# Performance work log

Hardware: AMD Instinct MI355X
Metric: run time of the kernel (lower is better)

The kernel has to match this reference:

```python
import jax, jax.numpy as jnp
import numpy as np

B, T, D = 2, 2048, 2048
H, HKV, RD = 16, 4, 64
DH = D // H          # 128
REP = H // HKV       # 4
NEG = -1e30


def _apply_rope(x, cos, sin, rd):
    # x: (B, h, T, Dh); cos/sin: (T, rd//2) broadcast over (B, h)
    xr, xp = x[..., :rd], x[..., rd:]
    x1, x2 = xr[..., ::2], xr[..., 1::2]
    rot = jnp.stack([x1 * cos - x2 * sin, x1 * sin + x2 * cos], axis=-1)
    rot = rot.reshape(x1.shape[:-1] + (rd,))
    return jnp.concatenate([rot, xp], axis=-1)


def setup_inputs() -> dict:
    key = jax.random.key(0)
    ks = jax.random.split(key, 6)
    x = jax.random.normal(ks[0], (B, T, D), dtype=jnp.float32)
    # rotary tables for the first RD dims (RD//2 frequency pairs)
    inv_freq = 1.0 / (10000.0 ** (np.arange(RD // 2, dtype=np.float32) / (RD // 2)))
    ang = np.arange(T, dtype=np.float32)[:, None] * inv_freq[None, :]  # (T, RD//2)
    cos = jnp.asarray(np.cos(ang), dtype=jnp.float32)
    sin = jnp.asarray(np.sin(ang), dtype=jnp.float32)
    s = 0.02
    Wq = jax.random.normal(ks[1], (H * DH, D), dtype=jnp.float32) * s
    Wk = jax.random.normal(ks[2], (HKV * DH, D), dtype=jnp.float32) * s
    Wv = jax.random.normal(ks[3], (HKV * DH, D), dtype=jnp.float32) * s
    Wo = jax.random.normal(ks[4], (D, D), dtype=jnp.float32) * s
    temp = jnp.full((H,), 1.0 / np.sqrt(DH), dtype=jnp.float32)
    return {"x": x, "cos": cos, "sin": sin, "Wq": Wq, "Wk": Wk, "Wv": Wv, "Wo": Wo, "temp": temp}


def reference(x, cos, sin, Wq, Wk, Wv, Wo, temp):
    Bt, Tt, _ = x.shape
    q = (x @ Wq.T).reshape(Bt, Tt, H, DH).transpose(0, 2, 1, 3)    # (B,H,T,Dh)
    k = (x @ Wk.T).reshape(Bt, Tt, HKV, DH).transpose(0, 2, 1, 3)  # (B,Hkv,T,Dh)
    v = (x @ Wv.T).reshape(Bt, Tt, HKV, DH).transpose(0, 2, 1, 3)
    k = jnp.repeat(k, REP, axis=1)  # GQA repeat_interleave -> (B,H,T,Dh)
    v = jnp.repeat(v, REP, axis=1)
    q = _apply_rope(q, cos, sin, RD)
    k = _apply_rope(k, cos, sin, RD)
    q = q * temp[None, :, None, None]
    # SDPA causal, with default 1/sqrt(Dh) scale on top of learned temp
    scores = jnp.einsum("bhqd,bhkd->bhqk", q, k) / np.sqrt(DH)
    causal = jnp.tril(jnp.ones((Tt, Tt), dtype=bool))
    scores = jnp.where(causal[None, None], scores, NEG)
    attn = jax.nn.softmax(scores, axis=-1)
    out = jnp.einsum("bhqk,bhkd->bhqd", attn, v)  # (B,H,T,Dh)
    out = out.transpose(0, 2, 1, 3).reshape(Bt, Tt, H * DH)
    return out @ Wo.T
```

## Files before the change

kernel.cpp:

```cpp
#include <hip/hip_runtime.h>
#include <hip/hip_bf16.h>
#include <math.h>

#define B_   2
#define T_   2048
#define D_   2048
#define H_   16
#define HKV_ 4
#define DH_  128
#define RD_  64
#define KD_  (HKV_ * DH_)
#define SQKV 3072
#define VOFF 2560

typedef __attribute__((ext_vector_type(8))) short  short8;
typedef __attribute__((ext_vector_type(4))) short  short4v;
typedef __attribute__((ext_vector_type(4))) float  floatx4;

__device__ __forceinline__ void async16(const __hip_bfloat16* g, __hip_bfloat16* l) {
  __builtin_amdgcn_global_load_lds(
      (const __attribute__((address_space(1))) void*)g,
      (__attribute__((address_space(3))) void*)l, 16, 0, 0);
}

__device__ __forceinline__ short bf16b(float x) {
  union { __hip_bfloat16 h; short s; } u;
  u.h = __float2bfloat16(x);
  return u.s;
}

struct ConvArgs {
  const float* src[5];
  __hip_bfloat16* dst[5];
  int n[5];
};

__global__ __launch_bounds__(256) void conv_bf16(ConvArgs a) {
  const int arr = blockIdx.y;
  const int i = (blockIdx.x * 256 + threadIdx.x) * 8;
  if (i >= a.n[arr]) return;
  const float4 f1 = *(const float4*)(a.src[arr] + i);
  const float4 f2 = *(const float4*)(a.src[arr] + i + 4);
  union { short8 v; __hip_bfloat16 h[8]; } o;
  o.h[0] = __float2bfloat16(f1.x); o.h[1] = __float2bfloat16(f1.y);
  o.h[2] = __float2bfloat16(f1.z); o.h[3] = __float2bfloat16(f1.w);
  o.h[4] = __float2bfloat16(f2.x); o.h[5] = __float2bfloat16(f2.y);
  o.h[6] = __float2bfloat16(f2.z); o.h[7] = __float2bfloat16(f2.w);
  *(short8*)(a.dst[arr] + i) = o.v;
}

template <int MODE>
__global__ __launch_bounds__(512, 2) void gemm_8ph(const __hip_bfloat16* __restrict__ A,
                                                   const __hip_bfloat16* __restrict__ Bw,
                                                   void* __restrict__ Cout,
                                                   __hip_bfloat16* __restrict__ vtout,
                                                   int M, int N, int K, int nwg_x) {
  __shared__ __hip_bfloat16 As[3][16 * 512];
  __shared__ __hip_bfloat16 Bs[3][16 * 512];

  const int tid  = threadIdx.x;
  const int lane = tid & 63;
  const int w    = tid >> 6;
  const int wm   = w >> 2, wn = w & 3;
  const int quad = lane >> 4, m16 = lane & 15;

  const int nwg = gridDim.x;
  const int q8  = nwg >> 3, r8 = nwg & 7;
  const int xcd = blockIdx.x & 7, o8 = blockIdx.x >> 3;
  const int swz = (xcd < r8 ? xcd * (q8 + 1) : r8 * (q8 + 1) + (xcd - r8) * q8) + o8;
  const int bx = swz % nwg_x, by = swz / nwg_x;
  const int bm = by * 256, bn = bx * 256;

  const int rl = m16;
  const int kc = quad;
  const __hip_bfloat16* gA0 = A  + (size_t)(bm + (w * 2 + 0) * 16 + rl) * K + kc * 8;
  const __hip_bfloat16* gA1 = A  + (size_t)(bm + (w * 2 + 1) * 16 + rl) * K + kc * 8;
  const __hip_bfloat16* gB0 = Bw + (size_t)(bn + (w * 2 + 0) * 16 + rl) * K + kc * 8;
  const __hip_bfloat16* gB1 = Bw + (size_t)(bn + (w * 2 + 1) * 16 + rl) * K + kc * 8;

  const int nt = K >> 5;

  async16(gA0,      &As[0][(w * 2 + 0) * 512]);
  async16(gA1,      &As[0][(w * 2 + 1) * 512]);
  async16(gB0,      &Bs[0][(w * 2 + 0) * 512]);
  async16(gB1,      &Bs[0][(w * 2 + 1) * 512]);
  async16(gA0 + 32, &As[1][(w * 2 + 0) * 512]);
  async16(gA1 + 32, &As[1][(w * 2 + 1) * 512]);
  async16(gB0 + 32, &Bs[1][(w * 2 + 0) * 512]);
  async16(gB1 + 32, &Bs[1][(w * 2 + 1) * 512]);

  floatx4 acc[8][4] = {};
  const int fragoff = (quad * 16 + m16) * 8;

  int cur = 0, stg = 2;
  for (int t = 0; t < nt; ++t) {
    if (t < nt - 1) asm volatile("s_waitcnt vmcnt(4)" ::: "memory");
    else            asm volatile("s_waitcnt vmcnt(0)" ::: "memory");
    __builtin_amdgcn_s_barrier();
    __builtin_amdgcn_sched_barrier(0);

    const __hip_bfloat16* abase = &As[cur][0];
    const __hip_bfloat16* bbase = &Bs[cur][0];
    const bool doStage = (t + 2 < nt);
    const size_t ko = (size_t)(t + 2) * 32;

    short8 a0[4], b[4];
#pragma unroll
    for (int i = 0; i < 4; ++i) {
      a0[i] = *(const short8*)(abase + (wm * 8 + i) * 512 + fragoff);
      b[i]  = *(const short8*)(bbase + (wn * 4 + i) * 512 + fragoff);
    }
    if (doStage) {
      async16(gA0 + ko, &As[stg][(w * 2 + 0) * 512]);
      async16(gA1 + ko, &As[stg][(w * 2 + 1) * 512]);
    }
    __builtin_amdgcn_s_barrier();
    __builtin_amdgcn_sched_barrier(0);
    __builtin_amdgcn_s_setprio(1);
#pragma unroll
    for (int i = 0; i < 4; ++i)
#pragma unroll
      for (int j = 0; j < 4; ++j)
        acc[i][j] = __builtin_amdgcn_mfma_f32_16x16x32_bf16(a0[i], b[j], acc[i][j], 0, 0, 0);
    __builtin_amdgcn_s_setprio(0);
    __builtin_amdgcn_s_barrier();
    __builtin_amdgcn_sched_barrier(0);

    short8 a1[4];
#pragma unroll
    for (int i = 0; i < 4; ++i)
      a1[i] = *(const short8*)(abase + (wm * 8 + 4 + i) * 512 + fragoff);
    if (doStage) {
      async16(gB0 + ko, &Bs[stg][(w * 2 + 0) * 512]);
      async16(gB1 + ko, &Bs[stg][(w * 2 + 1) * 512]);
    }
    __builtin_amdgcn_s_barrier();
    __builtin_amdgcn_sched_barrier(0);
    __builtin_amdgcn_s_setprio(1);
#pragma unroll
    for (int i = 0; i < 4; ++i)
#pragma unroll
      for (int j = 0; j < 4; ++j)
        acc[4 + i][j] = __builtin_amdgcn_mfma_f32_16x16x32_bf16(a1[i], b[j], acc[4 + i][j], 0, 0, 0);
    __builtin_amdgcn_s_setprio(0);

    cur = (cur == 2) ? 0 : cur + 1;
    stg = (stg == 2) ? 0 : stg + 1;
  }

  if (MODE == 2 && bn >= VOFF) {
#pragma unroll
    for (int mt = 0; mt < 8; ++mt)
#pragma unroll
      for (int j = 0; j < 4; ++j) {
        const int dh = bn + wn * 64 + j * 16 + m16 - VOFF;
        const int row0 = bm + wm * 128 + mt * 16 + quad * 4;
        const int bb = row0 >> 11, t0 = row0 & (T_ - 1);
        short4v pk;
#pragma unroll
        for (int reg = 0; reg < 4; ++reg) pk[reg] = bf16b(acc[mt][j][reg]);
        *(short4v*)&vtout[((size_t)(bb * HKV_ + (dh >> 7)) * DH_ + (dh & 127)) * T_ + t0] = pk;
      }
    return;
  }

#pragma unroll
  for (int mt = 0; mt < 8; ++mt)
#pragma unroll
    for (int j = 0; j < 4; ++j)
#pragma unroll
      for (int reg = 0; reg < 4; ++reg) {
        const int row = bm + wm * 128 + mt * 16 + quad * 4 + reg;
        const int col = bn + wn * 64 + j * 16 + m16;
        if (MODE == 0)
          ((float*)Cout)[(size_t)row * N + col] = acc[mt][j][reg];
        else
          ((__hip_bfloat16*)Cout)[(size_t)row * N + col] = __float2bfloat16(acc[mt][j][reg]);
      }
}

__global__ __launch_bounds__(512, 2) void gemm_k1(const __hip_bfloat16* __restrict__ A,
                                                  const __hip_bfloat16* __restrict__ Bw,
                                                  float* __restrict__ Cout,
                                                  int M, int N, int K, int nwg_x) {
  __shared__ __hip_bfloat16 As[3][8 * 512];
  __shared__ __hip_bfloat16 Bs[3][16 * 512];

  const int tid  = threadIdx.x;
  const int lane = tid & 63;
  const int w    = tid >> 6;
  const int wm   = w >> 2, wn = w & 3;
  const int quad = lane >> 4, m16 = lane & 15;

  const int nwg = gridDim.x;
  const int q8  = nwg >> 3, r8 = nwg & 7;
  const int xcd = blockIdx.x & 7, o8 = blockIdx.x >> 3;
  const int swz = (xcd < r8 ? xcd * (q8 + 1) : r8 * (q8 + 1) + (xcd - r8) * q8) + o8;
  const int bx = swz % nwg_x, by = swz / nwg_x;
  const int bm = by * 128, bn = bx * 256;

  const __hip_bfloat16* gA  = A  + (size_t)(bm + w * 16 + m16) * K + quad * 8;
  const __hip_bfloat16* gB0 = Bw + (size_t)(bn + (w * 2 + 0) * 16 + m16) * K + quad * 8;
  const __hip_bfloat16* gB1 = Bw + (size_t)(bn + (w * 2 + 1) * 16 + m16) * K + quad * 8;

  const int nt = K >> 5;

  async16(gA,       &As[0][w * 512]);
  async16(gB0,      &Bs[0][(w * 2 + 0) * 512]);
  async16(gB1,      &Bs[0][(w * 2 + 1) * 512]);
  async16(gA + 32,  &As[1][w * 512]);
  async16(gB0 + 32, &Bs[1][(w * 2 + 0) * 512]);
  async16(gB1 + 32, &Bs[1][(w * 2 + 1) * 512]);

  floatx4 acc[4][4] = {};
  const int fragoff = (quad * 16 + m16) * 8;

  int cur = 0, stg = 2;
  for (int t = 0; t < nt; ++t) {
    if (t < nt - 1) asm volatile("s_waitcnt vmcnt(3)" ::: "memory");
    else            asm volatile("s_waitcnt vmcnt(0)" ::: "memory");
    __builtin_amdgcn_s_barrier();
    __builtin_amdgcn_sched_barrier(0);

    const __hip_bfloat16* abase = &As[cur][0];
    const __hip_bfloat16* bbase = &Bs[cur][0];

    short8 a[4], b[4];
#pragma unroll
    for (int i = 0; i < 4; ++i) {
      a[i] = *(const short8*)(abase + (wm * 4 + i) * 512 + fragoff);
      b[i] = *(const short8*)(bbase + (wn * 4 + i) * 512 + fragoff);
    }
    if (t + 2 < nt) {
      const size_t ko = (size_t)(t + 2) * 32;
      async16(gA + ko,  &As[stg][w * 512]);
      async16(gB0 + ko, &Bs[stg][(w * 2 + 0) * 512]);
      async16(gB1 + ko, &Bs[stg][(w * 2 + 1) * 512]);
    }
    __builtin_amdgcn_s_setprio(1);
#pragma unroll
    for (int i = 0; i < 4; ++i)
#pragma unroll
      for (int j = 0; j < 4; ++j)
        acc[i][j] = __builtin_amdgcn_mfma_f32_16x16x32_bf16(a[i], b[j], acc[i][j], 0, 0, 0);
    __builtin_amdgcn_s_setprio(0);

    cur = (cur == 2) ? 0 : cur + 1;
    stg = (stg == 2) ? 0 : stg + 1;
  }

#pragma unroll
  for (int mi = 0; mi < 4; ++mi)
#pragma unroll
    for (int nj = 0; nj < 4; ++nj)
#pragma unroll
      for (int reg = 0; reg < 4; ++reg) {
        const int row = bm + wm * 64 + mi * 16 + quad * 4 + reg;
        const int col = bn + wn * 64 + nj * 16 + m16;
        Cout[(size_t)row * N + col] = acc[mi][nj][reg];
      }
}

__global__ __launch_bounds__(256) void rope_qk(__hip_bfloat16* __restrict__ qkv,
                                               const float* __restrict__ cosT,
                                               const float* __restrict__ sinT,
                                               const float* __restrict__ temp,
                                               float inv_sqrt_dh) {
  const int unit = blockIdx.x * 4 + (threadIdx.x >> 6);
  const int lane = threadIdx.x & 63;
  const int M = B_ * T_;
  int bt, off;
  float scale;
  if (unit < M * H_) {
    const int h = unit % H_;
    bt = unit / H_;
    off = h * DH_;
    scale = temp[h] * inv_sqrt_dh * 1.44269504088896340736f;
  } else {
    const int u2 = unit - M * H_;
    const int h = u2 % HKV_;
    bt = u2 / HKV_;
    off = D_ + h * DH_;
    scale = 1.0f;
  }
  const int t = bt & (T_ - 1);
  __hip_bfloat16* p = qkv + (size_t)bt * SQKV + off;
  if (lane < 32) {
    const float x1 = __bfloat162float(p[2 * lane]);
    const float x2 = __bfloat162float(p[2 * lane + 1]);
    const float c = cosT[t * (RD_ / 2) + lane];
    const float s = sinT[t * (RD_ / 2) + lane];
    p[2 * lane]     = __float2bfloat16((x1 * c - x2 * s) * scale);
    p[2 * lane + 1] = __float2bfloat16((x1 * s + x2 * c) * scale);
  } else {
    const int d0 = RD_ + (lane - 32) * 2;
    p[d0]     = __float2bfloat16(__bfloat162float(p[d0]) * scale);
    p[d0 + 1] = __float2bfloat16(__bfloat162float(p[d0 + 1]) * scale);
  }
}

__global__ __launch_bounds__(256, 2) void flash_attn_t2(
    const __hip_bfloat16* __restrict__ qkv,
    const __hip_bfloat16* __restrict__ vt,
    __hip_bfloat16* __restrict__ ao) {
  __shared__ __hip_bfloat16 Ks[2][8192];
  __shared__ __hip_bfloat16 Vs[2][8192];

  const int tid = threadIdx.x, lane = tid & 63, w = tid >> 6;
  const int quad = lane >> 4, m16 = lane & 15;

  const int bid = blockIdx.x;
  const int g = bid & 7;
  const int b = g >> 2, kvh = g & 3;
  const int u = bid >> 3;
  const int qt = 63 - u;
  const int h = kvh * 4 + w;
  const int qRow0 = qt * 32;
  const int ktEnd = (qt >> 1) + 1;

  const size_t bT = (size_t)b * T_;

  short8 qa[2][4];
#pragma unroll
  for (int qi = 0; qi < 2; qi++) {
    const __hip_bfloat16* qp = qkv + (bT + qRow0 + qi * 16 + m16) * SQKV + h * DH_;
#pragma unroll
    for (int ks = 0; ks < 4; ks++) qa[qi][ks] = *(const short8*)(qp + ks * 32 + quad * 8);
  }

  const short one = (short)0x3F80;
  const short4v ones4 = {one, one, one, one};

  const __hip_bfloat16* kptr[4];
  const __hip_bfloat16* vptr[4];
#pragma unroll
  for (int e = 0; e < 4; e++) {
    const int I = w * 4 + e;
    const int panelK = I >> 2, kcK = (I & 3) * 4 + quad;
    kptr[e] = qkv + D_ + (bT + panelK * 16 + m16) * SQKV + kvh * DH_ + kcK * 8;
    const int panelV = I >> 1, tc = (I & 1) * 4 + quad;
    vptr[e] = vt + ((size_t)(b * HKV_ + kvh) * DH_ + panelV * 16 + m16) * T_ + tc * 8;
  }

#pragma unroll
  for (int e = 0; e < 4; e++) {
    const int I = w * 4 + e;
    async16(kptr[e], &Ks[0][I * 512]);
    async16(vptr[e], &Vs[0][I * 512]);
    kptr[e] += (size_t)64 * SQKV;
    vptr[e] += 64;
  }

  floatx4 ot[8][2] = {};
  floatx4 lt[2] = {};

  for (int kt = 0; kt < ktEnd; kt++) {
    const int cur = kt & 1;
    __syncthreads();
    if (kt + 1 < ktEnd) {
      const int nxt = cur ^ 1;
#pragma unroll
      for (int e = 0; e < 4; e++) {
        const int I = w * 4 + e;
        async16(kptr[e], &Ks[nxt][I * 512]);
        async16(vptr[e], &Vs[nxt][I * 512]);
        kptr[e] += (size_t)64 * SQKV;
        vptr[e] += 64;
      }
    }

    floatx4 st[4][2] = {};
#pragma unroll
    for (int ki = 0; ki < 4; ki++)
#pragma unroll
      for (int ks = 0; ks < 4; ks++) {
        const int unit = ki * 256 + (ks * 4 + quad) * 16 + m16;
        const short8 kf = *(const short8*)&Ks[cur][unit * 8];
#pragma unroll
        for (int qi = 0; qi < 2; qi++)
          st[ki][qi] = __builtin_amdgcn_mfma_f32_16x16x32_bf16(kf, qa[qi][ks],
                                                               st[ki][qi], 0, 0, 0);
      }

    if (kt == ktEnd - 1) {
#pragma unroll
      for (int ki = 0; ki < 4; ki++)
#pragma unroll
        for (int qi = 0; qi < 2; qi++) {
          const int rowg = qRow0 + qi * 16 + m16;
#pragma unroll
          for (int reg = 0; reg < 4; reg++) {
            const int keyg = kt * 64 + ki * 16 + quad * 4 + reg;
            if (keyg > rowg) st[ki][qi][reg] = -1e30f;
          }
        }
    }

    short4v pf[4][2];
#pragma unroll
    for (int ki = 0; ki < 4; ki++)
#pragma unroll
      for (int qi = 0; qi < 2; qi++) {
        short4v t;
#pragma unroll
        for (int reg = 0; reg < 4; reg++) t[reg] = bf16b(exp2f(st[ki][qi][reg]));
        pf[ki][qi] = t;
      }

#pragma unroll
    for (int mi = 0; mi < 8; mi++)
#pragma unroll
      for (int ki = 0; ki < 4; ki++) {
        const int unit = mi * 128 + (ki * 2 + (quad >> 1)) * 16 + m16;
        const short4v vf = *(const short4v*)&Vs[cur][unit * 8 + (quad & 1) * 4];
#pragma unroll
        for (int qi = 0; qi < 2; qi++)
          ot[mi][qi] = __builtin_amdgcn_mfma_f32_16x16x16bf16_1k(vf, pf[ki][qi],
                                                                 ot[mi][qi], 0, 0, 0);
      }
#pragma unroll
    for (int ki = 0; ki < 4; ki++)
#pragma unroll
      for (int qi = 0; qi < 2; qi++)
        lt[qi] = __builtin_amdgcn_mfma_f32_16x16x16bf16_1k(ones4, pf[ki][qi],
                                                           lt[qi], 0, 0, 0);
  }

#pragma unroll
  for (int qi = 0; qi < 2; qi++) {
    const float inv = 1.0f / lt[qi][0];
    const size_t gr = (bT + qRow0 + qi * 16 + m16) * D_ + h * DH_;
#pragma unroll
    for (int mi = 0; mi < 8; mi++) {
      short4v o;
#pragma unroll
      for (int reg = 0; reg < 4; reg++) o[reg] = bf16b(ot[mi][qi][reg] * inv);
      *(short4v*)&ao[gr + mi * 16 + quad * 4] = o;
    }
  }
}

extern "C" void kernel_launch(void* const* d_in, const int* in_sizes, int n_in,
                              void* d_out, int out_size, void* d_ws, size_t ws_size,
                              hipStream_t stream) {
  const float* x    = (const float*)d_in[0];
  const float* cosT = (const float*)d_in[1];
  const float* sinT = (const float*)d_in[2];
  const float* Wq   = (const float*)d_in[3];
  const float* Wk   = (const float*)d_in[4];
  const float* Wv   = (const float*)d_in[5];
  const float* Wo   = (const float*)d_in[6];
  const float* temp = (const float*)d_in[7];
  float* out = (float*)d_out;

  const int M = B_ * T_;
  const size_t XN   = (size_t)M * D_;
  const size_t WQN  = (size_t)D_ * D_;
  const size_t WKN  = (size_t)KD_ * D_;
  const size_t QKVN = (size_t)M * SQKV;
  const size_t KN   = (size_t)M * KD_;

  __hip_bfloat16* ws = (__hip_bfloat16*)d_ws;
  __hip_bfloat16* xb    = ws;  ws += XN;
  __hip_bfloat16* wqkvb = ws;  ws += WQN + 2 * WKN;
  __hip_bfloat16* wob   = ws;  ws += WQN;
  __hip_bfloat16* qkvb  = ws;  ws += QKVN;
  __hip_bfloat16* vtb   = ws;  ws += KN;
  __hip_bfloat16* aob   = ws;  ws += XN;

  dim3 blk(256);

  ConvArgs ca;
  ca.src[0] = x;  ca.dst[0] = xb;                  ca.n[0] = (int)XN;
  ca.src[1] = Wq; ca.dst[1] = wqkvb;               ca.n[1] = (int)WQN;
  ca.src[2] = Wk; ca.dst[2] = wqkvb + WQN;         ca.n[2] = (int)WKN;
  ca.src[3] = Wv; ca.dst[3] = wqkvb + WQN + WKN;   ca.n[3] = (int)WKN;
  ca.src[4] = Wo; ca.dst[4] = wob;                 ca.n[4] = (int)WQN;
  conv_bf16<<<dim3(4096, 5), blk, 0, stream>>>(ca);

  gemm_8ph<2><<<dim3((SQKV / 256) * (M / 256)), dim3(512), 0, stream>>>(
      xb, wqkvb, qkvb, vtb, M, SQKV, D_, SQKV / 256);

  const float inv_sqrt_dh = 1.0f / sqrtf((float)DH_);
  rope_qk<<<(M * (H_ + HKV_)) / 4, blk, 0, stream>>>(qkvb, cosT, sinT, temp, inv_sqrt_dh);

  flash_attn_t2<<<512, blk, 0, stream>>>(qkvb, vtb, aob);

  gemm_k1<<<dim3((D_ / 256) * (M / 128)), dim3(512), 0, stream>>>(
      aob, wob, out, M, D_, D_, D_ / 256);
}
```

Before: 354.0 us.

## Split flash attention query rows across 512 threads, one 16-row slice per wave

The flash attention block grows from 4 to 8 waves, and each wave now handles a single 16-row query slice for one head instead of two. Per-wave accumulator and register use drop by half, and each wave issues half as many K/V async loads into shared memory. The log2e factor moves out of the Q scaling, and exp2f is replaced by __expf, which is equivalent maths. The trade-off is more waves per block competing for the same LDS tiles, more barrier participants, and possibly lower occupancy per CU because of launch_bounds(512,2).

```diff
diff --git a/kernel.cpp b/kernel.cpp
--- a/kernel.cpp
+++ b/kernel.cpp
@@ -275,7 +275,7 @@
     const int h = unit % H_;
     bt = unit / H_;
     off = h * DH_;
-    scale = temp[h] * inv_sqrt_dh * 1.44269504088896340736f;
+    scale = temp[h] * inv_sqrt_dh;
   } else {
     const int u2 = unit - M * H_;
     const int h = u2 % HKV_;
@@ -299,7 +299,7 @@
   }
 }
 
-__global__ __launch_bounds__(256, 2) void flash_attn_t2(
+__global__ __launch_bounds__(512, 2) void flash_attn_t2(
     const __hip_bfloat16* __restrict__ qkv,
     const __hip_bfloat16* __restrict__ vt,
     __hip_bfloat16* __restrict__ ao) {
@@ -314,28 +314,28 @@
   const int b = g >> 2, kvh = g & 3;
   const int u = bid >> 3;
   const int qt = 63 - u;
-  const int h = kvh * 4 + w;
-  const int qRow0 = qt * 32;
+  const int h = kvh * 4 + (w & 3);
+  const int qsub = w >> 2;
+  const int qRow0 = qt * 32 + qsub * 16;
   const int ktEnd = (qt >> 1) + 1;
 
   const size_t bT = (size_t)b * T_;
 
-  short8 qa[2][4];
-#pragma unroll
-  for (int qi = 0; qi < 2; qi++) {
-    const __hip_bfloat16* qp = qkv + (bT + qRow0 + qi * 16 + m16) * SQKV + h * DH_;
-#pragma unroll
-    for (int ks = 0; ks < 4; ks++) qa[qi][ks] = *(const short8*)(qp + ks * 32 + quad * 8);
+  short8 qa[4];
+  {
+    const __hip_bfloat16* qp = qkv + (bT + qRow0 + m16) * SQKV + h * DH_;
+#pragma unroll
+    for (int ks = 0; ks < 4; ks++) qa[ks] = *(const short8*)(qp + ks * 32 + quad * 8);
   }
 
   const short one = (short)0x3F80;
   const short4v ones4 = {one, one, one, one};
 
-  const __hip_bfloat16* kptr[4];
-  const __hip_bfloat16* vptr[4];
-#pragma unroll
-  for (int e = 0; e < 4; e++) {
-    const int I = w * 4 + e;
+  const __hip_bfloat16* kptr[2];
+  const __hip_bfloat16* vptr[2];
+#pragma unroll
+  for (int e = 0; e < 2; e++) {
+    const int I = w * 2 + e;
     const int panelK = I >> 2, kcK = (I & 3) * 4 + quad;
     kptr[e] = qkv + D_ + (bT + panelK * 16 + m16) * SQKV + kvh * DH_ + kcK * 8;
     const int panelV = I >> 1, tc = (I & 1) * 4 + quad;
@@ -343,16 +343,16 @@
   }
 
 #pragma unroll
-  for (int e = 0; e < 4; e++) {
-    const int I = w * 4 + e;
+  for (int e = 0; e < 2; e++) {
+    const int I = w * 2 + e;
     async16(kptr[e], &Ks[0][I * 512]);
     async16(vptr[e], &Vs[0][I * 512]);
     kptr[e] += (size_t)64 * SQKV;
     vptr[e] += 64;
   }
 
-  floatx4 ot[8][2] = {};
-  floatx4 lt[2] = {};
+  floatx4 ot[8] = {};
+  floatx4 lt = {};
 
   for (int kt = 0; kt < ktEnd; kt++) {
     const int cur = kt & 1;
@@ -360,8 +360,8 @@
     if (kt + 1 < ktEnd) {
       const int nxt = cur ^ 1;
 #pragma unroll
-      for (int e = 0; e < 4; e++) {
-        const int I = w * 4 + e;
+      for (int e = 0; e < 2; e++) {
+        const int I = w * 2 + e;
         async16(kptr[e], &Ks[nxt][I * 512]);
         async16(vptr[e], &Vs[nxt][I * 512]);
         kptr[e] += (size_t)64 * SQKV;
@@ -369,43 +369,35 @@
       }
     }
 
-    floatx4 st[4][2] = {};
+    floatx4 st[4] = {};
 #pragma unroll
     for (int ki = 0; ki < 4; ki++)
 #pragma unroll
       for (int ks = 0; ks < 4; ks++) {
         const int unit = ki * 256 + (ks * 4 + quad) * 16 + m16;
         const short8 kf = *(const short8*)&Ks[cur][unit * 8];
-#pragma unroll
-        for (int qi = 0; qi < 2; qi++)
-          st[ki][qi] = __builtin_amdgcn_mfma_f32_16x16x32_bf16(kf, qa[qi][ks],
-                                                               st[ki][qi], 0, 0, 0);
+        st[ki] = __builtin_amdgcn_mfma_f32_16x16x32_bf16(kf, qa[ks], st[ki], 0, 0, 0);
       }
 
     if (kt == ktEnd - 1) {
+      const int rowg = qRow0 + m16;
 #pragma unroll
       for (int ki = 0; ki < 4; ki++)
 #pragma unroll
-        for (int qi = 0; qi < 2; qi++) {
-          const int rowg = qRow0 + qi * 16 + m16;
-#pragma unroll
-          for (int reg = 0; reg < 4; reg++) {
-            const int keyg = kt * 64 + ki * 16 + quad * 4 + reg;
-            if (keyg > rowg) st[ki][qi][reg] = -1e30f;
-          }
+        for (int reg = 0; reg < 4; reg++) {
+          const int keyg = kt * 64 + ki * 16 + quad * 4 + reg;
+          if (keyg > rowg) st[ki][reg] = -1e30f;
         }
     }
 
-    short4v pf[4][2];
-#pragma unroll
-    for (int ki = 0; ki < 4; ki++)
-#pragma unroll
-      for (int qi = 0; qi < 2; qi++) {
-        short4v t;
-#pragma unroll
-        for (int reg = 0; reg < 4; reg++) t[reg] = bf16b(exp2f(st[ki][qi][reg]));
-        pf[ki][qi] = t;
-      }
+    short4v pf[4];
+#pragma unroll
+    for (int ki = 0; ki < 4; ki++) {
+      short4v t;
+#pragma unroll
+      for (int reg = 0; reg < 4; reg++) t[reg] = bf16b(__expf(st[ki][reg]));
+      pf[ki] = t;
+    }
 
 #pragma unroll
     for (int mi = 0; mi < 8; mi++)
@@ -413,28 +405,21 @@
       for (int ki = 0; ki < 4; ki++) {
         const int unit = mi * 128 + (ki * 2 + (quad >> 1)) * 16 + m16;
         const short4v vf = *(const short4v*)&Vs[cur][unit * 8 + (quad & 1) * 4];
-#pragma unroll
-        for (int qi = 0; qi < 2; qi++)
-          ot[mi][qi] = __builtin_amdgcn_mfma_f32_16x16x16bf16_1k(vf, pf[ki][qi],
-                                                                 ot[mi][qi], 0, 0, 0);
+        ot[mi] = __builtin_amdgcn_mfma_f32_16x16x16bf16_1k(vf, pf[ki], ot[mi], 0, 0, 0);
       }
 #pragma unroll
     for (int ki = 0; ki < 4; ki++)
-#pragma unroll
-      for (int qi = 0; qi < 2; qi++)
-        lt[qi] = __builtin_amdgcn_mfma_f32_16x16x16bf16_1k(ones4, pf[ki][qi],
-                                                           lt[qi], 0, 0, 0);
-  }
-
-#pragma unroll
-  for (int qi = 0; qi < 2; qi++) {
-    const float inv = 1.0f / lt[qi][0];
-    const size_t gr = (bT + qRow0 + qi * 16 + m16) * D_ + h * DH_;
+      lt = __builtin_amdgcn_mfma_f32_16x16x16bf16_1k(ones4, pf[ki], lt, 0, 0, 0);
+  }
+
+  {
+    const float inv = 1.0f / lt[0];
+    const size_t gr = (bT + qRow0 + m16) * D_ + h * DH_;
 #pragma unroll
     for (int mi = 0; mi < 8; mi++) {
       short4v o;
 #pragma unroll
-      for (int reg = 0; reg < 4; reg++) o[reg] = bf16b(ot[mi][qi][reg] * inv);
+      for (int reg = 0; reg < 4; reg++) o[reg] = bf16b(ot[mi][reg] * inv);
       *(short4v*)&ao[gr + mi * 16 + quad * 4] = o;
     }
   }
@@ -484,7 +469,7 @@
   const float inv_sqrt_dh = 1.0f / sqrtf((float)DH_);
   rope_qk<<<(M * (H_ + HKV_)) / 4, blk, 0, stream>>>(qkvb, cosT, sinT, temp, inv_sqrt_dh);
 
-  flash_attn_t2<<<512, blk, 0, stream>>>(qkvb, vtb, aob);
+  flash_attn_t2<<<512, dim3(512), 0, stream>>>(qkvb, vtb, aob);
 
   gemm_k1<<<dim3((D_ / 256) * (M / 128)), dim3(512), 0, stream>>>(
       aob, wob, out, M, D_, D_, D_ / 256);
```

After: 344.3 us. 1.03x faster.
